# Performance work log

Measured on AMD Instinct MI355X. Metric: run time of the kernel, lower is better.

The kernel has to match this reference:

```python
import jax, jax.numpy as jnp
import numpy as np

L, HID, NH, NKV, HD, INTER = 16, 960, 15, 5, 64, 2560
VOCAB, NV, NT, PRE, SD = 49152, 192, 48, 241, 32
THETA, EPS, B = 100000.0, 1e-5, 16
GROUPS = NH // NKV


def setup_inputs() -> dict:
    key = jax.random.key(0)
    ks = jax.random.split(key, 20)
    s = 0.02
    rn = lambda k, shp: jax.random.normal(k, shp, jnp.float32) * s
    return {
        'vision_features': jax.random.normal(ks[0], (B, NV, HID), jnp.float32),
        'lang_token_ids': jax.random.randint(ks[1], (B, NT), 0, VOCAB),
        'lang_mask': jnp.ones((B, NT), dtype=bool),
        'state': jax.random.normal(ks[2], (B, SD), jnp.float32),
        'embed': rn(ks[3], (VOCAB, HID)),
        'state_w': rn(ks[4], (SD, HID)),
        'state_b': jnp.zeros((HID,), jnp.float32),
        'Wq': rn(ks[5], (L, HID, NH * HD)),
        'Wk': rn(ks[6], (L, HID, NKV * HD)),
        'Wv': rn(ks[7], (L, HID, NKV * HD)),
        'Wo': rn(ks[8], (L, NH * HD, HID)),
        'Wg': rn(ks[9], (L, HID, INTER)),
        'Wu': rn(ks[10], (L, HID, INTER)),
        'Wd': rn(ks[11], (L, INTER, HID)),
        'ln1': jnp.ones((L, HID), jnp.float32),
        'ln2': jnp.ones((L, HID), jnp.float32),
    }


def _rms(x, w):
    var = jnp.mean(jnp.square(x), axis=-1, keepdims=True)
    return x * jax.lax.rsqrt(var + EPS) * w


def _rotate_half(x):
    h = x.shape[-1] // 2
    return jnp.concatenate([-x[..., h:], x[..., :h]], axis=-1)


def _rope_tables(position_ids):
    # position_ids: [B, S] -> cos/sin: [B, S, HD]
    inv_freq = 1.0 / (THETA ** (jnp.arange(0, HD, 2, dtype=jnp.float32) / HD))
    freqs = position_ids.astype(jnp.float32)[..., None] * inv_freq  # [B,S,HD/2]
    emb = jnp.concatenate([freqs, freqs], axis=-1)
    return jnp.cos(emb), jnp.sin(emb)


def _apply_rope(x, cos, sin):
    # x: [B,S,H,D]; cos/sin: [B,S,D]
    return x * cos[:, :, None, :] + _rotate_half(x) * sin[:, :, None, :]


def _attention(q, k, v, mask2d):
    # q: [B,S,NH,HD]; k,v: [B,S,NKV,HD]; mask2d: [B,S,S] bool (query i, key j)
    kx = jnp.repeat(k, GROUPS, axis=2)  # GQA expand -> [B,S,NH,HD]
    vx = jnp.repeat(v, GROUPS, axis=2)
    scores = jnp.einsum('bihd,bjhd->bhij', q, kx) * (HD ** -0.5)
    big_neg = jnp.finfo(jnp.float32).min
    scores = jnp.where(mask2d[:, None, :, :], scores, big_neg)
    probs = jax.nn.softmax(scores, axis=-1)
    out = jnp.einsum('bhij,bjhd->bihd', probs, vx)
    return out.reshape(q.shape[0], q.shape[1], NH * HD)


def reference(vision_features, lang_token_ids, lang_mask, state,
              embed, state_w, state_b, Wq, Wk, Wv, Wo, Wg, Wu, Wd, ln1, ln2):
    lang_emb = embed[lang_token_ids] * jnp.sqrt(jnp.float32(HID))  # [B,NT,HID]
    state_emb = (state @ state_w + state_b)[:, None, :]            # [B,1,HID]
    x = jnp.concatenate([vision_features, lang_emb, state_emb], axis=1)  # [B,PRE,HID]

    pad = jnp.concatenate([jnp.ones((B, NV), bool), lang_mask.astype(bool),
                           jnp.ones((B, 1), bool)], axis=1)  # [B,PRE]
    position_ids = jnp.clip(jnp.cumsum(pad.astype(jnp.int32), axis=1) - 1, 0, None)
    cos, sin = _rope_tables(position_ids)

    att_marks = jnp.zeros((PRE,), jnp.int32).at[NV + NT:].set(1)
    cum = jnp.cumsum(att_marks)
    att2d = cum[None, :] >= cum[:, None]  # [S_q, S_kv]: key cum <= query cum
    pad2d = pad[:, :, None] & pad[:, None, :]
    mask2d = att2d[None, :, :] & pad2d  # [B,S,S]

    def layer(x, w):
        h = _rms(x, w['ln1'])
        S = h.shape[1]
        q = (h @ w['Wq']).reshape(B, S, NH, HD)
        k = (h @ w['Wk']).reshape(B, S, NKV, HD)
        v = (h @ w['Wv']).reshape(B, S, NKV, HD)
        q = _apply_rope(q, cos, sin)
        k = _apply_rope(k, cos, sin)
        a = _attention(q, k, v, mask2d)
        x = x + a @ w['Wo']
        h2 = _rms(x, w['ln2'])
        m = (jax.nn.silu(h2 @ w['Wg']) * (h2 @ w['Wu'])) @ w['Wd']
        return x + m, (k, v)

    weights = {'Wq': Wq, 'Wk': Wk, 'Wv': Wv, 'Wo': Wo,
               'Wg': Wg, 'Wu': Wu, 'Wd': Wd, 'ln1': ln1, 'ln2': ln2}
    _, (keys, values) = jax.lax.scan(layer, x, weights)
    # keys/values: [L, B, PRE, NKV, HD]
    return keys, values
```

## Files before the change

### kernel.cpp

```cpp
#include <hip/hip_runtime.h>
#include <hip/hip_bf16.h>

namespace {

typedef __bf16 bf16_t;
typedef __bf16 bf16x8 __attribute__((ext_vector_type(8)));
typedef __bf16 bf16x4 __attribute__((ext_vector_type(4)));
typedef float f32x4 __attribute__((ext_vector_type(4)));

constexpr int kL     = 16;
constexpr int kHid   = 960;
constexpr int kNH    = 15;
constexpr int kNKV   = 5;
constexpr int kHD    = 64;
constexpr int kInter = 2560;
constexpr int kNV    = 192;
constexpr int kNT    = 48;
constexpr int kPre   = 241;
constexpr int kSD    = 32;
constexpr int kB     = 16;
constexpr int kTok   = kB * kPre;
constexpr int kTokP  = 3968;
constexpr int kQKV   = 1600;
constexpr float kEps = 1e-5f;
constexpr float kSqrtHid = 30.98386677f;

constexpr size_t kWoOff     = (size_t)1664 * 960;
constexpr size_t kWgOff     = kWoOff + (size_t)1024 * 960;
constexpr size_t kWuOff     = kWgOff + (size_t)2560 * 960;
constexpr size_t kWdOff     = kWuOff + (size_t)2560 * 960;
constexpr size_t kWPerLayer = kWdOff + (size_t)1024 * 2560;

__device__ __forceinline__ void gload16(const bf16_t* g, bf16_t* l) {
  __builtin_amdgcn_global_load_lds((const __attribute__((address_space(1))) void*)g,
                                   (__attribute__((address_space(3))) void*)l, 16, 0, 0);
}

__global__ void build_x_kernel(const float* __restrict__ vision,
                               const int*   __restrict__ tokens,
                               const float* __restrict__ state,
                               const float* __restrict__ embed,
                               const float* __restrict__ sw,
                               const float* __restrict__ sb,
                               float* __restrict__ x) {
  int idx = blockIdx.x * blockDim.x + threadIdx.x;
  if (idx >= kTok * kHid) return;
  int t = idx / kHid, c = idx - t * kHid;
  int b = t / kPre, s = t - b * kPre;
  float v;
  if (s < kNV) {
    v = vision[((size_t)b * kNV + s) * kHid + c];
  } else if (s < kNV + kNT) {
    int tok = tokens[b * kNT + (s - kNV)];
    v = embed[(size_t)tok * kHid + c] * kSqrtHid;
  } else {
    float acc = sb[c];
#pragma unroll
    for (int i = 0; i < kSD; ++i) acc += state[b * kSD + i] * sw[i * kHid + c];
    v = acc;
  }
  x[idx] = v;
}

__global__ void rope_table_kernel(float* __restrict__ cosT, float* __restrict__ sinT) {
  int idx = blockIdx.x * blockDim.x + threadIdx.x;
  if (idx >= kPre * 32) return;
  int s = idx >> 5, fi = idx & 31;
  float inv = __expf(-(2.0f * (float)fi / (float)kHD) * __logf(100000.0f));
  float fr = (float)s * inv;
  cosT[idx] = cosf(fr);
  sinT[idx] = sinf(fr);
}

__device__ void transpose_tile(const float* __restrict__ src, bf16_t* __restrict__ dst,
                               int K, int N, int tile) {
  __shared__ float ts[64][65];
  int ntn = N >> 6;
  int tk = tile / ntn, tn = tile - tk * ntn;
  int t = threadIdx.x;
  int r = t >> 2, c0 = (t & 3) << 4;
  const float* sp = src + (size_t)((tk << 6) + r) * N + (tn << 6) + c0;
  float4 a = ((const float4*)sp)[0];
  float4 b = ((const float4*)sp)[1];
  float4 c = ((const float4*)sp)[2];
  float4 d = ((const float4*)sp)[3];
  ts[r][c0 + 0] = a.x;  ts[r][c0 + 1] = a.y;  ts[r][c0 + 2] = a.z;  ts[r][c0 + 3] = a.w;
  ts[r][c0 + 4] = b.x;  ts[r][c0 + 5] = b.y;  ts[r][c0 + 6] = b.z;  ts[r][c0 + 7] = b.w;
  ts[r][c0 + 8] = c.x;  ts[r][c0 + 9] = c.y;  ts[r][c0 +10] = c.z;  ts[r][c0 +11] = c.w;
  ts[r][c0 +12] = d.x;  ts[r][c0 +13] = d.y;  ts[r][c0 +14] = d.z;  ts[r][c0 +15] = d.w;
  __syncthreads();
  bf16_t* dp = dst + (size_t)((tn << 6) + r) * K + (tk << 6) + c0;
  bf16x8 o0, o1;
#pragma unroll
  for (int i = 0; i < 8; ++i) o0[i] = (bf16_t)ts[c0 + i][r];
#pragma unroll
  for (int i = 0; i < 8; ++i) o1[i] = (bf16_t)ts[c0 + 8 + i][r];
  *(bf16x8*)dp = o0;
  *(bf16x8*)(dp + 8) = o1;
}

__global__ __launch_bounds__(256)
void wconv_kernel(const float* __restrict__ Wq, const float* __restrict__ Wk,
                  const float* __restrict__ Wv, const float* __restrict__ Wo,
                  const float* __restrict__ Wg, const float* __restrict__ Wu,
                  const float* __restrict__ Wd, bf16_t* __restrict__ wall) {
  int bid = blockIdx.x;
  int l = bid / 2400, t = bid - l * 2400;
  bf16_t* wl = wall + (size_t)l * kWPerLayer;
  if      (t < 225)  transpose_tile(Wq + (size_t)l * 921600, wl, 960, 960, t);
  else if (t < 300)  transpose_tile(Wk + (size_t)l * 307200, wl + (size_t)960 * 960, 960, 320, t - 225);
  else if (t < 375)  transpose_tile(Wv + (size_t)l * 307200, wl + (size_t)1280 * 960, 960, 320, t - 300);
  else if (t < 600)  transpose_tile(Wo + (size_t)l * 921600, wl + kWoOff, 960, 960, t - 375);
  else if (t < 1200) transpose_tile(Wg + (size_t)l * 2457600, wl + kWgOff, 960, 2560, t - 600);
  else if (t < 1800) transpose_tile(Wu + (size_t)l * 2457600, wl + kWuOff, 960, 2560, t - 1200);
  else               transpose_tile(Wd + (size_t)l * 2457600, wl + kWdOff, 2560, 960, t - 1800);
}

__global__ __launch_bounds__(256)
void rmsnorm_bf16_kernel(const float* __restrict__ x, const float* __restrict__ w,
                         bf16_t* __restrict__ h) {
  int t = blockIdx.x;
  int tid = threadIdx.x;
  const float* xr = x + (size_t)t * kHid;
  float4 v = make_float4(0.f, 0.f, 0.f, 0.f);
  if (tid < 240) v = ((const float4*)xr)[tid];
  float ss = v.x * v.x + v.y * v.y + v.z * v.z + v.w * v.w;
#pragma unroll
  for (int off = 32; off; off >>= 1) ss += __shfl_xor(ss, off);
  __shared__ float part[4];
  if ((tid & 63) == 0) part[tid >> 6] = ss;
  __syncthreads();
  float tot = part[0] + part[1] + part[2] + part[3];
  float scale = rsqrtf(tot * (1.f / (float)kHid) + kEps);
  if (tid < 240) {
    float4 wv = ((const float4*)w)[tid];
    bf16x4 o;
    o[0] = (bf16_t)(v.x * scale * wv.x);
    o[1] = (bf16_t)(v.y * scale * wv.y);
    o[2] = (bf16_t)(v.z * scale * wv.z);
    o[3] = (bf16_t)(v.w * scale * wv.w);
    *(bf16x4*)&h[(size_t)t * kHid + tid * 4] = o;
  }
}


__global__ __launch_bounds__(256, 4)
void gemm_qkv_kernel(const bf16_t* __restrict__ A, const bf16_t* __restrict__ Bt,
                     bf16_t* __restrict__ qkv, float* __restrict__ outk,
                     float* __restrict__ outv,
                     const float* __restrict__ cosT, const float* __restrict__ sinT) {
  constexpr int K = kHid;
  constexpr int NT = K / 32;
  __shared__ alignas(16) bf16_t As[2][4096];
  __shared__ alignas(16) bf16_t Bs[2][2048];
  int tid = threadIdx.x;
  int m0 = blockIdx.y * 128, n0 = blockIdx.x * 64;
  int lane = tid & 63, wid = tid >> 6;
  int wr = wid * 32;
  int r0 = tid >> 2, c0 = (tid & 3) * 8;
  int lr = lane & 15, lg = lane >> 4;

  const bf16_t* a0 = A + (size_t)(m0 + r0) * K + c0;
  const bf16_t* a1 = a0 + (size_t)64 * K;
  const bf16_t* b0 = Bt + (size_t)(n0 + r0) * K + c0;

  f32x4 acc[2][4];
#pragma unroll
  for (int m = 0; m < 2; ++m)
#pragma unroll
    for (int n = 0; n < 4; ++n) acc[m][n] = (f32x4){0.f, 0.f, 0.f, 0.f};

  int arow0 = (wr + lr) * 32 + lg * 8;
  int brow0 = lr * 32 + lg * 8;

  gload16(a0, &As[0][tid * 8]);
  gload16(a1, &As[0][2048 + tid * 8]);
  if (r0 < 64) gload16(b0, &Bs[0][tid * 8]);
  __syncthreads();

  int cur = 0;
  for (int t = 0; t < NT; ++t) {
    if (t + 1 < NT) {
      int k1 = (t + 1) * 32;
      gload16(a0 + k1, &As[cur ^ 1][tid * 8]);
      gload16(a1 + k1, &As[cur ^ 1][2048 + tid * 8]);
      gload16(b0 + k1, &Bs[cur ^ 1][tid * 8]);
    }
    bf16x8 af[2], bfr[4];
#pragma unroll
    for (int m = 0; m < 2; ++m) af[m] = *(const bf16x8*)&As[cur][arow0 + m * 16 * 32];
#pragma unroll
    for (int n = 0; n < 4; ++n) bfr[n] = *(const bf16x8*)&Bs[cur][brow0 + n * 16 * 32];
#pragma unroll
    for (int m = 0; m < 2; ++m)
#pragma unroll
      for (int n = 0; n < 4; ++n)
        acc[m][n] = __builtin_amdgcn_mfma_f32_16x16x32_bf16(af[m], bfr[n], acc[m][n], 0, 0, 0);
    __syncthreads();
    cur ^= 1;
  }

  int cbase = n0;
  int cr4 = lg * 4;
  if (cbase < 1280) {
    bool isQ = cbase < 960;
    float scale = isQ ? 0.125f : 1.0f;
#pragma unroll
    for (int m = 0; m < 2; ++m) {
      int row = m0 + wr + m * 16 + cr4;
#pragma unroll
      for (int r = 0; r < 4; ++r) {
        int rr = row + r;
        if (rr >= kTok) continue;
        int s = rr % kPre;
        bf16_t* qrow = qkv + (size_t)rr * kQKV + cbase;
        float* krow = outk + (size_t)rr * 320 + (cbase - 960);
#pragma unroll
        for (int n = 0; n < 2; ++n) {
          int d = n * 16 + lr;
          float c = cosT[s * 32 + d], sn = sinT[s * 32 + d];
          float lo = acc[m][n][r], hi = acc[m][n + 2][r];
          float y0 = lo * c - hi * sn;
          float y1 = hi * c + lo * sn;
          qrow[d]      = (bf16_t)(y0 * scale);
          qrow[d + 32] = (bf16_t)(y1 * scale);
          if (!isQ) { krow[d] = y0; krow[d + 32] = y1; }
        }
      }
    }
  } else {
#pragma unroll
    for (int m = 0; m < 2; ++m) {
      int row = m0 + wr + m * 16 + cr4;
#pragma unroll
      for (int r = 0; r < 4; ++r) {
        int rr = row + r;
        if (rr >= kTok) continue;
        bf16_t* qrow = qkv + (size_t)rr * kQKV + cbase;
        float* vrow = outv + (size_t)rr * 320 + (cbase - 1280);
#pragma unroll
        for (int n = 0; n < 4; ++n) {
          int d = n * 16 + lr;
          float v = acc[m][n][r];
          qrow[d] = (bf16_t)v;
          vrow[d] = v;
        }
      }
    }
  }
}

__global__ __launch_bounds__(256, 4)
void gemm_res_kernel(const bf16_t* __restrict__ A, const bf16_t* __restrict__ Bt,
                     const float* __restrict__ src, float* __restrict__ C,
                     int M, int N, int K) {
  __shared__ alignas(16) bf16_t As[2][4096];
  __shared__ alignas(16) bf16_t Bs[2][2048];
  int tid = threadIdx.x;
  int m0 = blockIdx.y * 128, n0 = blockIdx.x * 64;
  int lane = tid & 63, wid = tid >> 6;
  int wr = wid * 32;
  int r0 = tid >> 2, c0 = (tid & 3) * 8;
  int lr = lane & 15, lg = lane >> 4;

  const bf16_t* a0 = A + (size_t)(m0 + r0) * K + c0;
  const bf16_t* a1 = a0 + (size_t)64 * K;
  const bf16_t* b0 = Bt + (size_t)(n0 + r0) * K + c0;

  f32x4 acc[2][4];
#pragma unroll
  for (int m = 0; m < 2; ++m)
#pragma unroll
    for (int n = 0; n < 4; ++n) acc[m][n] = (f32x4){0.f, 0.f, 0.f, 0.f};

  int arow0 = (wr + lr) * 32 + lg * 8;
  int brow0 = lr * 32 + lg * 8;

  gload16(a0, &As[0][tid * 8]);
  gload16(a1, &As[0][2048 + tid * 8]);
  gload16(b0, &Bs[0][tid * 8]);
  __syncthreads();

  int NT = K / 32;
  int cur = 0;
  for (int t = 0; t < NT; ++t) {
    if (t + 1 < NT) {
      int k1 = (t + 1) * 32;
      gload16(a0 + k1, &As[cur ^ 1][tid * 8]);
      gload16(a1 + k1, &As[cur ^ 1][2048 + tid * 8]);
      gload16(b0 + k1, &Bs[cur ^ 1][tid * 8]);
    }
    bf16x8 af[2], bfr[4];
#pragma unroll
    for (int m = 0; m < 2; ++m) af[m] = *(const bf16x8*)&As[cur][arow0 + m * 16 * 32];
#pragma unroll
    for (int n = 0; n < 4; ++n) bfr[n] = *(const bf16x8*)&Bs[cur][brow0 + n * 16 * 32];
#pragma unroll
    for (int m = 0; m < 2; ++m)
#pragma unroll
      for (int n = 0; n < 4; ++n)
        acc[m][n] = __builtin_amdgcn_mfma_f32_16x16x32_bf16(af[m], bfr[n], acc[m][n], 0, 0, 0);
    __syncthreads();
    cur ^= 1;
  }

  int cr4 = lg * 4;
#pragma unroll
  for (int m = 0; m < 2; ++m) {
    int row = m0 + wr + m * 16 + cr4;
#pragma unroll
    for (int n = 0; n < 4; ++n) {
      int col = n0 + n * 16 + lr;
#pragma unroll
      for (int r = 0; r < 4; ++r) {
        int rr = row + r;
        if (rr < M) {
          size_t off = (size_t)rr * N + col;
          C[off] = src[off] + acc[m][n][r];
        }
      }
    }
  }
}

__global__ __launch_bounds__(256)
void gemm_dual_kernel(const bf16_t* __restrict__ A, const bf16_t* __restrict__ Bg,
                      const bf16_t* __restrict__ Bu, bf16_t* __restrict__ act,
                      int M, int K) {
  __shared__ alignas(16) bf16_t As[2][4096];
  __shared__ alignas(16) bf16_t Gs[2][2048];
  __shared__ alignas(16) bf16_t Us[2][2048];
  int tid = threadIdx.x;
  int m0 = blockIdx.y * 128, n0 = blockIdx.x * 64;
  int lane = tid & 63, wid = tid >> 6;
  int wr = wid * 32;
  int r0 = tid >> 2, c0 = (tid & 3) * 8;
  int lr = lane & 15, lg = lane >> 4;

  const bf16_t* a0 = A + (size_t)(m0 + r0) * K + c0;
  const bf16_t* a1 = a0 + (size_t)64 * K;
  const bf16_t* g0 = Bg + (size_t)(n0 + r0) * K + c0;
  const bf16_t* u0 = Bu + (size_t)(n0 + r0) * K + c0;

  f32x4 accg[2][4], accu[2][4];
#pragma unroll
  for (int m = 0; m < 2; ++m)
#pragma unroll
    for (int n = 0; n < 4; ++n) {
      accg[m][n] = (f32x4){0.f, 0.f, 0.f, 0.f};
      accu[m][n] = (f32x4){0.f, 0.f, 0.f, 0.f};
    }

  int arow0 = (wr + lr) * 32 + lg * 8;
  int brow0 = lr * 32 + lg * 8;

  gload16(a0, &As[0][tid * 8]);
  gload16(a1, &As[0][2048 + tid * 8]);
  gload16(g0, &Gs[0][tid * 8]);
  gload16(u0, &Us[0][tid * 8]);
  __syncthreads();

  int NT = K / 32;
  int cur = 0;
  for (int t = 0; t < NT; ++t) {
    if (t + 1 < NT) {
      int k1 = (t + 1) * 32;
      gload16(a0 + k1, &As[cur ^ 1][tid * 8]);
      gload16(a1 + k1, &As[cur ^ 1][2048 + tid * 8]);
      gload16(g0 + k1, &Gs[cur ^ 1][tid * 8]);
      gload16(u0 + k1, &Us[cur ^ 1][tid * 8]);
    }
    bf16x8 af[2], bfr[4];
#pragma unroll
    for (int m = 0; m < 2; ++m) af[m] = *(const bf16x8*)&As[cur][arow0 + m * 16 * 32];
#pragma unroll
    for (int n = 0; n < 4; ++n) bfr[n] = *(const bf16x8*)&Gs[cur][brow0 + n * 16 * 32];
#pragma unroll
    for (int m = 0; m < 2; ++m)
#pragma unroll
      for (int n = 0; n < 4; ++n)
        accg[m][n] = __builtin_amdgcn_mfma_f32_16x16x32_bf16(af[m], bfr[n], accg[m][n], 0, 0, 0);
#pragma unroll
    for (int n = 0; n < 4; ++n) bfr[n] = *(const bf16x8*)&Us[cur][brow0 + n * 16 * 32];
#pragma unroll
    for (int m = 0; m < 2; ++m)
#pragma unroll
      for (int n = 0; n < 4; ++n)
        accu[m][n] = __builtin_amdgcn_mfma_f32_16x16x32_bf16(af[m], bfr[n], accu[m][n], 0, 0, 0);
    __syncthreads();
    cur ^= 1;
  }

  int cr4 = lg * 4;
#pragma unroll
  for (int m = 0; m < 2; ++m) {
    int row = m0 + wr + m * 16 + cr4;
#pragma unroll
    for (int n = 0; n < 4; ++n) {
      int col = n0 + n * 16 + lr;
#pragma unroll
      for (int r = 0; r < 4; ++r) {
        int rr = row + r;
        if (rr < M) {
          float g = accg[m][n][r];
          float u = accu[m][n][r];
          float silu = g / (1.f + __expf(-g));
          act[(size_t)rr * kInter + col] = (bf16_t)(silu * u);
        }
      }
    }
  }
}

__global__ __launch_bounds__(256)
void attn_mfma_kernel(const bf16_t* __restrict__ qkv, bf16_t* __restrict__ aout) {
  int h = blockIdx.x, b = blockIdx.y;
  int kvh = h / 3;
  constexpr int LDK = 72;
  constexpr int LDV = 264;
  __shared__ alignas(16) bf16_t Ks[256 * LDK];
  __shared__ alignas(16) bf16_t Vt[64 * LDV];
  __shared__ alignas(16) bf16_t Ps[4][16 * LDV];
  const bf16_t* base = qkv + (size_t)b * kPre * kQKV;
  int tid = threadIdx.x;
  for (int i = tid; i < 2048; i += 256) {
    int j = i >> 3, c = (i & 7) * 8;
    bf16x8 k8, v8;
    if (j < kPre) {
      k8 = *(const bf16x8*)(base + (size_t)j * kQKV + 960 + kvh * 64 + c);
      v8 = *(const bf16x8*)(base + (size_t)j * kQKV + 1280 + kvh * 64 + c);
    } else {
#pragma unroll
      for (int e = 0; e < 8; ++e) { k8[e] = (bf16_t)0.f; v8[e] = (bf16_t)0.f; }
    }
    *(bf16x8*)&Ks[j * LDK + c] = k8;
#pragma unroll
    for (int e = 0; e < 8; ++e) Vt[(c + e) * LDV + j] = v8[e];
  }
  __syncthreads();
  int wid = tid >> 6, lane = tid & 63;
  int lr = lane & 15, lg = lane >> 4;
  bf16_t* myP = &Ps[wid][0];
  for (int qt = wid * 4; qt < wid * 4 + 4; ++qt) {
    int q0 = qt * 16;
    int qrow = q0 + lr; if (qrow > 240) qrow = 240;
    const bf16_t* qp = base + (size_t)qrow * kQKV + h * 64 + lg * 8;
    bf16x8 aq0 = *(const bf16x8*)qp;
    bf16x8 aq1 = *(const bf16x8*)(qp + 32);
    f32x4 sacc[16];
#pragma unroll
    for (int ct = 0; ct < 16; ++ct) sacc[ct] = (f32x4){0.f, 0.f, 0.f, 0.f};
#pragma unroll
    for (int ct = 0; ct < 16; ++ct) {
      int key = ct * 16 + lr;
      bf16x8 kb0 = *(const bf16x8*)&Ks[key * LDK + lg * 8];
      sacc[ct] = __builtin_amdgcn_mfma_f32_16x16x32_bf16(aq0, kb0, sacc[ct], 0, 0, 0);
      bf16x8 kb1 = *(const bf16x8*)&Ks[key * LDK + 32 + lg * 8];
      sacc[ct] = __builtin_amdgcn_mfma_f32_16x16x32_bf16(aq1, kb1, sacc[ct], 0, 0, 0);
    }
    float rmax[4] = {-1e30f, -1e30f, -1e30f, -1e30f};
#pragma unroll
    for (int ct = 0; ct < 16; ++ct) {
      int j = ct * 16 + lr;
#pragma unroll
      for (int r = 0; r < 4; ++r) {
        int q = q0 + lg * 4 + r;
        bool ok = (q < 240) ? (j < kPre) : (j == 240);
        float s = ok ? sacc[ct][r] : -1e30f;
        sacc[ct][r] = s;
        rmax[r] = fmaxf(rmax[r], s);
      }
    }
#pragma unroll
    for (int off = 8; off; off >>= 1) {
#pragma unroll
      for (int r = 0; r < 4; ++r) rmax[r] = fmaxf(rmax[r], __shfl_xor(rmax[r], off));
    }
    float rsum[4] = {0.f, 0.f, 0.f, 0.f};
#pragma unroll
    for (int ct = 0; ct < 16; ++ct) {
#pragma unroll
      for (int r = 0; r < 4; ++r) {
        float s = sacc[ct][r];
        float e = (s > -1e29f) ? __expf(s - rmax[r]) : 0.f;
        rsum[r] += e;
        myP[(lg * 4 + r) * LDV + ct * 16 + lr] = (bf16_t)e;
      }
    }
#pragma unroll
    for (int off = 8; off; off >>= 1) {
#pragma unroll
      for (int r = 0; r < 4; ++r) rsum[r] += __shfl_xor(rsum[r], off);
    }
    f32x4 oacc[4];
#pragma unroll
    for (int dt = 0; dt < 4; ++dt) oacc[dt] = (f32x4){0.f, 0.f, 0.f, 0.f};
#pragma unroll
    for (int ks = 0; ks < 8; ++ks) {
      bf16x8 pa = *(const bf16x8*)&myP[lr * LDV + ks * 32 + lg * 8];
#pragma unroll
      for (int dt = 0; dt < 4; ++dt) {
        bf16x8 vbf = *(const bf16x8*)&Vt[(dt * 16 + lr) * LDV + ks * 32 + lg * 8];
        oacc[dt] = __builtin_amdgcn_mfma_f32_16x16x32_bf16(pa, vbf, oacc[dt], 0, 0, 0);
      }
    }
    float linv[4];
#pragma unroll
    for (int r = 0; r < 4; ++r) linv[r] = 1.f / rsum[r];
#pragma unroll
    for (int dt = 0; dt < 4; ++dt) {
#pragma unroll
      for (int r = 0; r < 4; ++r) {
        int q = q0 + lg * 4 + r;
        if (q < kPre) {
          aout[((size_t)b * kPre + q) * kHid + h * 64 + dt * 16 + lr] =
              (bf16_t)(oacc[dt][r] * linv[r]);
        }
      }
    }
  }
}

}

extern "C" void kernel_launch(void* const* d_in, const int* in_sizes, int n_in,
                              void* d_out, int out_size, void* d_ws, size_t ws_size,
                              hipStream_t stream) {
  const float* vision = (const float*)d_in[0];
  const int*   tokens = (const int*)d_in[1];
  const float* state = (const float*)d_in[3];
  const float* embed = (const float*)d_in[4];
  const float* sw    = (const float*)d_in[5];
  const float* sb    = (const float*)d_in[6];
  const float* Wq    = (const float*)d_in[7];
  const float* Wk    = (const float*)d_in[8];
  const float* Wv    = (const float*)d_in[9];
  const float* Wo    = (const float*)d_in[10];
  const float* Wg    = (const float*)d_in[11];
  const float* Wu    = (const float*)d_in[12];
  const float* Wd    = (const float*)d_in[13];
  const float* ln1   = (const float*)d_in[14];
  const float* ln2   = (const float*)d_in[15];

  char* w = (char*)d_ws;
  float*  x      = (float*)w;   w += (size_t)kTok * kHid * 4;
  bf16_t* qkv    = (bf16_t*)w;  w += (size_t)kTok * kQKV * 2;
  bf16_t* h_bf   = (bf16_t*)w;  w += (size_t)kTokP * kHid * 2;
  bf16_t* a_bf   = (bf16_t*)w;  w += (size_t)kTokP * kHid * 2;
  bf16_t* act_bf = (bf16_t*)w;  w += (size_t)kTokP * kInter * 2;
  bf16_t* wall   = (bf16_t*)w;  w += kWPerLayer * kL * 2;
  float*  cosT   = (float*)w;   w += (size_t)kPre * 32 * 4;
  float*  sinT   = (float*)w;   w += (size_t)kPre * 32 * 4;

  float* out_k = (float*)d_out;
  float* out_v = out_k + (size_t)kL * kTok * 320;

  build_x_kernel<<<(kTok * kHid + 255) / 256, 256, 0, stream>>>(
      vision, tokens, state, embed, sw, sb, x);
  rope_table_kernel<<<(kPre * 32 + 255) / 256, 256, 0, stream>>>(cosT, sinT);
  wconv_kernel<<<2400 * kL, 256, 0, stream>>>(Wq, Wk, Wv, Wo, Wg, Wu, Wd, wall);

  for (int l = 0; l < kL; ++l) {
    bf16_t* wl = wall + (size_t)l * kWPerLayer;
    rmsnorm_bf16_kernel<<<kTok, 256, 0, stream>>>(x, ln1 + (size_t)l * kHid, h_bf);
    gemm_qkv_kernel<<<dim3(25, 31), 256, 0, stream>>>(
        h_bf, wl, qkv, out_k + (size_t)l * kTok * 320, out_v + (size_t)l * kTok * 320,
        cosT, sinT);
    attn_mfma_kernel<<<dim3(15, 16), 256, 0, stream>>>(qkv, a_bf);
    gemm_res_kernel<<<dim3(15, 31), 256, 0, stream>>>(
        a_bf, wl + kWoOff, x, x, kTok, kHid, kHid);
    rmsnorm_bf16_kernel<<<kTok, 256, 0, stream>>>(x, ln2 + (size_t)l * kHid, h_bf);
    gemm_dual_kernel<<<dim3(40, 31), 256, 0, stream>>>(
        h_bf, wl + kWgOff, wl + kWuOff, act_bf, kTok, kHid);
    gemm_res_kernel<<<dim3(15, 31), 256, 0, stream>>>(
        act_bf, wl + kWdOff, x, x, kTok, kHid, kInter);
  }
}
```

Before: 3.543 ms.

## Fuse RMSNorm into GEMM prologues using atomically accumulated row sum-of-squares

Removes the standalone rmsnorm kernels. The residual GEMMs now accumulate per-row sums of squares with atomics in their epilogue, and the QKV and gate/up GEMMs read fp32 x directly and apply the norm scale and weight while staging A tiles into shared memory. This saves two launches and the bf16 h round-trip per layer. In exchange the GEMMs load fp32 A (twice the bytes) through registers instead of direct-to-LDS loads, recompute the normalisation in each column block, and add atomic traffic plus a memset.

```diff
diff --git a/kernel.cpp b/kernel.cpp
--- a/kernel.cpp
+++ b/kernel.cpp
@@ -34,6 +34,15 @@
 __device__ __forceinline__ void gload16(const bf16_t* g, bf16_t* l) {
   __builtin_amdgcn_global_load_lds((const __attribute__((address_space(1))) void*)g,
                                    (__attribute__((address_space(3))) void*)l, 16, 0, 0);
+}
+
+__device__ __forceinline__ bf16x8 pack8(float4 a, float4 b, float4 wa, float4 wb, float s) {
+  bf16x8 o;
+  o[0] = (bf16_t)(a.x * s * wa.x); o[1] = (bf16_t)(a.y * s * wa.y);
+  o[2] = (bf16_t)(a.z * s * wa.z); o[3] = (bf16_t)(a.w * s * wa.w);
+  o[4] = (bf16_t)(b.x * s * wb.x); o[5] = (bf16_t)(b.y * s * wb.y);
+  o[6] = (bf16_t)(b.z * s * wb.z); o[7] = (bf16_t)(b.w * s * wb.w);
+  return o;
 }
 
 __global__ void build_x_kernel(const float* __restrict__ vision,
@@ -62,6 +71,22 @@
   x[idx] = v;
 }
 
+__global__ __launch_bounds__(256)
+void rowssq_kernel(const float* __restrict__ x, float* __restrict__ ssq) {
+  int t = blockIdx.x;
+  int tid = threadIdx.x;
+  const float* xr = x + (size_t)t * kHid;
+  float4 v = make_float4(0.f, 0.f, 0.f, 0.f);
+  if (tid < 240) v = ((const float4*)xr)[tid];
+  float ss = v.x * v.x + v.y * v.y + v.z * v.z + v.w * v.w;
+#pragma unroll
+  for (int off = 32; off; off >>= 1) ss += __shfl_xor(ss, off);
+  __shared__ float part[4];
+  if ((tid & 63) == 0) part[tid >> 6] = ss;
+  __syncthreads();
+  if (tid == 0) ssq[t] = part[0] + part[1] + part[2] + part[3];
+}
+
 __global__ void rope_table_kernel(float* __restrict__ cosT, float* __restrict__ sinT) {
   int idx = blockIdx.x * blockDim.x + threadIdx.x;
   if (idx >= kPre * 32) return;
@@ -116,36 +141,10 @@
   else               transpose_tile(Wd + (size_t)l * 2457600, wl + kWdOff, 2560, 960, t - 1800);
 }
 
+
 __global__ __launch_bounds__(256)
-void rmsnorm_bf16_kernel(const float* __restrict__ x, const float* __restrict__ w,
-                         bf16_t* __restrict__ h) {
-  int t = blockIdx.x;
-  int tid = threadIdx.x;
-  const float* xr = x + (size_t)t * kHid;
-  float4 v = make_float4(0.f, 0.f, 0.f, 0.f);
-  if (tid < 240) v = ((const float4*)xr)[tid];
-  float ss = v.x * v.x + v.y * v.y + v.z * v.z + v.w * v.w;
-#pragma unroll
-  for (int off = 32; off; off >>= 1) ss += __shfl_xor(ss, off);
-  __shared__ float part[4];
-  if ((tid & 63) == 0) part[tid >> 6] = ss;
-  __syncthreads();
-  float tot = part[0] + part[1] + part[2] + part[3];
-  float scale = rsqrtf(tot * (1.f / (float)kHid) + kEps);
-  if (tid < 240) {
-    float4 wv = ((const float4*)w)[tid];
-    bf16x4 o;
-    o[0] = (bf16_t)(v.x * scale * wv.x);
-    o[1] = (bf16_t)(v.y * scale * wv.y);
-    o[2] = (bf16_t)(v.z * scale * wv.z);
-    o[3] = (bf16_t)(v.w * scale * wv.w);
-    *(bf16x4*)&h[(size_t)t * kHid + tid * 4] = o;
-  }
-}
-
-
-__global__ __launch_bounds__(256, 4)
-void gemm_qkv_kernel(const bf16_t* __restrict__ A, const bf16_t* __restrict__ Bt,
+void gemm_qkv_kernel(const float* __restrict__ X, const float* __restrict__ ssq,
+                     const float* __restrict__ lnw, const bf16_t* __restrict__ Bt,
                      bf16_t* __restrict__ qkv, float* __restrict__ outk,
                      float* __restrict__ outv,
                      const float* __restrict__ cosT, const float* __restrict__ sinT) {
@@ -160,9 +159,12 @@
   int r0 = tid >> 2, c0 = (tid & 3) * 8;
   int lr = lane & 15, lg = lane >> 4;
 
-  const bf16_t* a0 = A + (size_t)(m0 + r0) * K + c0;
-  const bf16_t* a1 = a0 + (size_t)64 * K;
-  const bf16_t* b0 = Bt + (size_t)(n0 + r0) * K + c0;
+  const float* xa = X + (size_t)(m0 + r0) * K + c0;
+  const float* xb = xa + (size_t)64 * K;
+  const bf16_t* gb = Bt + (size_t)(n0 + r0) * K + c0;
+
+  float sc0 = rsqrtf(ssq[m0 + r0] * (1.f / 960.f) + kEps);
+  float sc1 = rsqrtf(ssq[m0 + r0 + 64] * (1.f / 960.f) + kEps);
 
   f32x4 acc[2][4];
 #pragma unroll
@@ -173,18 +175,26 @@
   int arow0 = (wr + lr) * 32 + lg * 8;
   int brow0 = lr * 32 + lg * 8;
 
-  gload16(a0, &As[0][tid * 8]);
-  gload16(a1, &As[0][2048 + tid * 8]);
-  if (r0 < 64) gload16(b0, &Bs[0][tid * 8]);
+  {
+    float4 a0 = *(const float4*)xa, a1 = *(const float4*)(xa + 4);
+    float4 b0 = *(const float4*)xb, b1 = *(const float4*)(xb + 4);
+    float4 w0 = *(const float4*)(lnw + c0), w1 = *(const float4*)(lnw + c0 + 4);
+    *(bf16x8*)&As[0][tid * 8] = pack8(a0, a1, w0, w1, sc0);
+    *(bf16x8*)&As[0][2048 + tid * 8] = pack8(b0, b1, w0, w1, sc1);
+    gload16(gb, &Bs[0][tid * 8]);
+  }
   __syncthreads();
 
   int cur = 0;
   for (int t = 0; t < NT; ++t) {
-    if (t + 1 < NT) {
+    float4 a0, a1, b0, b1, w0, w1;
+    bool pf = (t + 1 < NT);
+    if (pf) {
       int k1 = (t + 1) * 32;
-      gload16(a0 + k1, &As[cur ^ 1][tid * 8]);
-      gload16(a1 + k1, &As[cur ^ 1][2048 + tid * 8]);
-      gload16(b0 + k1, &Bs[cur ^ 1][tid * 8]);
+      a0 = *(const float4*)(xa + k1); a1 = *(const float4*)(xa + k1 + 4);
+      b0 = *(const float4*)(xb + k1); b1 = *(const float4*)(xb + k1 + 4);
+      w0 = *(const float4*)(lnw + k1 + c0); w1 = *(const float4*)(lnw + k1 + c0 + 4);
+      gload16(gb + k1, &Bs[cur ^ 1][tid * 8]);
     }
     bf16x8 af[2], bfr[4];
 #pragma unroll
@@ -196,6 +206,10 @@
 #pragma unroll
       for (int n = 0; n < 4; ++n)
         acc[m][n] = __builtin_amdgcn_mfma_f32_16x16x32_bf16(af[m], bfr[n], acc[m][n], 0, 0, 0);
+    if (pf) {
+      *(bf16x8*)&As[cur ^ 1][tid * 8] = pack8(a0, a1, w0, w1, sc0);
+      *(bf16x8*)&As[cur ^ 1][2048 + tid * 8] = pack8(b0, b1, w0, w1, sc1);
+    }
     __syncthreads();
     cur ^= 1;
   }
@@ -253,7 +267,7 @@
 __global__ __launch_bounds__(256, 4)
 void gemm_res_kernel(const bf16_t* __restrict__ A, const bf16_t* __restrict__ Bt,
                      const float* __restrict__ src, float* __restrict__ C,
-                     int M, int N, int K) {
+                     float* __restrict__ ssq_out, int M, int N, int K) {
   __shared__ alignas(16) bf16_t As[2][4096];
   __shared__ alignas(16) bf16_t Bs[2][2048];
   int tid = threadIdx.x;
@@ -305,6 +319,7 @@
   }
 
   int cr4 = lg * 4;
+  float ps[2][4] = {};
 #pragma unroll
   for (int m = 0; m < 2; ++m) {
     int row = m0 + wr + m * 16 + cr4;
@@ -316,15 +331,35 @@
         int rr = row + r;
         if (rr < M) {
           size_t off = (size_t)rr * N + col;
-          C[off] = src[off] + acc[m][n][r];
+          float val = src[off] + acc[m][n][r];
+          C[off] = val;
+          ps[m][r] += val * val;
         }
       }
     }
   }
+#pragma unroll
+  for (int m = 0; m < 2; ++m)
+#pragma unroll
+    for (int r = 0; r < 4; ++r) {
+#pragma unroll
+      for (int off = 8; off; off >>= 1) ps[m][r] += __shfl_xor(ps[m][r], off);
+    }
+  if (lr == 0) {
+#pragma unroll
+    for (int m = 0; m < 2; ++m) {
+#pragma unroll
+      for (int r = 0; r < 4; ++r) {
+        int rr = m0 + wr + m * 16 + cr4 + r;
+        if (rr < M) atomicAdd(&ssq_out[rr], ps[m][r]);
+      }
+    }
+  }
 }
 
 __global__ __launch_bounds__(256)
-void gemm_dual_kernel(const bf16_t* __restrict__ A, const bf16_t* __restrict__ Bg,
+void gemm_dual_kernel(const float* __restrict__ X, const float* __restrict__ ssq,
+                      const float* __restrict__ lnw, const bf16_t* __restrict__ Bg,
                       const bf16_t* __restrict__ Bu, bf16_t* __restrict__ act,
                       int M, int K) {
   __shared__ alignas(16) bf16_t As[2][4096];
@@ -337,10 +372,13 @@
   int r0 = tid >> 2, c0 = (tid & 3) * 8;
   int lr = lane & 15, lg = lane >> 4;
 
-  const bf16_t* a0 = A + (size_t)(m0 + r0) * K + c0;
-  const bf16_t* a1 = a0 + (size_t)64 * K;
+  const float* xa = X + (size_t)(m0 + r0) * K + c0;
+  const float* xb = xa + (size_t)64 * K;
   const bf16_t* g0 = Bg + (size_t)(n0 + r0) * K + c0;
   const bf16_t* u0 = Bu + (size_t)(n0 + r0) * K + c0;
+
+  float sc0 = rsqrtf(ssq[m0 + r0] * (1.f / 960.f) + kEps);
+  float sc1 = rsqrtf(ssq[m0 + r0 + 64] * (1.f / 960.f) + kEps);
 
   f32x4 accg[2][4], accu[2][4];
 #pragma unroll
@@ -354,19 +392,27 @@
   int arow0 = (wr + lr) * 32 + lg * 8;
   int brow0 = lr * 32 + lg * 8;
 
-  gload16(a0, &As[0][tid * 8]);
-  gload16(a1, &As[0][2048 + tid * 8]);
-  gload16(g0, &Gs[0][tid * 8]);
-  gload16(u0, &Us[0][tid * 8]);
+  {
+    float4 a0 = *(const float4*)xa, a1 = *(const float4*)(xa + 4);
+    float4 b0 = *(const float4*)xb, b1 = *(const float4*)(xb + 4);
+    float4 w0 = *(const float4*)(lnw + c0), w1 = *(const float4*)(lnw + c0 + 4);
+    *(bf16x8*)&As[0][tid * 8] = pack8(a0, a1, w0, w1, sc0);
+    *(bf16x8*)&As[0][2048 + tid * 8] = pack8(b0, b1, w0, w1, sc1);
+    gload16(g0, &Gs[0][tid * 8]);
+    gload16(u0, &Us[0][tid * 8]);
+  }
   __syncthreads();
 
   int NT = K / 32;
   int cur = 0;
   for (int t = 0; t < NT; ++t) {
-    if (t + 1 < NT) {
+    float4 a0, a1, b0, b1, w0, w1;
+    bool pf = (t + 1 < NT);
+    if (pf) {
       int k1 = (t + 1) * 32;
-      gload16(a0 + k1, &As[cur ^ 1][tid * 8]);
-      gload16(a1 + k1, &As[cur ^ 1][2048 + tid * 8]);
+      a0 = *(const float4*)(xa + k1); a1 = *(const float4*)(xa + k1 + 4);
+      b0 = *(const float4*)(xb + k1); b1 = *(const float4*)(xb + k1 + 4);
+      w0 = *(const float4*)(lnw + k1 + c0); w1 = *(const float4*)(lnw + k1 + c0 + 4);
       gload16(g0 + k1, &Gs[cur ^ 1][tid * 8]);
       gload16(u0 + k1, &Us[cur ^ 1][tid * 8]);
     }
@@ -387,6 +433,10 @@
 #pragma unroll
       for (int n = 0; n < 4; ++n)
         accu[m][n] = __builtin_amdgcn_mfma_f32_16x16x32_bf16(af[m], bfr[n], accu[m][n], 0, 0, 0);
+    if (pf) {
+      *(bf16x8*)&As[cur ^ 1][tid * 8] = pack8(a0, a1, w0, w1, sc0);
+      *(bf16x8*)&As[cur ^ 1][2048 + tid * 8] = pack8(b0, b1, w0, w1, sc1);
+    }
     __syncthreads();
     cur ^= 1;
   }
@@ -543,36 +593,41 @@
   const float* ln2   = (const float*)d_in[15];
 
   char* w = (char*)d_ws;
-  float*  x      = (float*)w;   w += (size_t)kTok * kHid * 4;
+  float*  x      = (float*)w;   w += (size_t)kTokP * kHid * 4;
   bf16_t* qkv    = (bf16_t*)w;  w += (size_t)kTok * kQKV * 2;
-  bf16_t* h_bf   = (bf16_t*)w;  w += (size_t)kTokP * kHid * 2;
   bf16_t* a_bf   = (bf16_t*)w;  w += (size_t)kTokP * kHid * 2;
   bf16_t* act_bf = (bf16_t*)w;  w += (size_t)kTokP * kInter * 2;
   bf16_t* wall   = (bf16_t*)w;  w += kWPerLayer * kL * 2;
   float*  cosT   = (float*)w;   w += (size_t)kPre * 32 * 4;
   float*  sinT   = (float*)w;   w += (size_t)kPre * 32 * 4;
+  float*  ssqA   = (float*)w;   w += (size_t)(kL + 1) * kTokP * 4;
+  float*  ssqB   = (float*)w;   w += (size_t)kL * kTokP * 4;
 
   float* out_k = (float*)d_out;
   float* out_v = out_k + (size_t)kL * kTok * 320;
 
+  hipMemsetAsync(ssqA, 0, (size_t)(2 * kL + 1) * kTokP * 4, stream);
+
   build_x_kernel<<<(kTok * kHid + 255) / 256, 256, 0, stream>>>(
       vision, tokens, state, embed, sw, sb, x);
+  rowssq_kernel<<<kTok, 256, 0, stream>>>(x, ssqA);
   rope_table_kernel<<<(kPre * 32 + 255) / 256, 256, 0, stream>>>(cosT, sinT);
   wconv_kernel<<<2400 * kL, 256, 0, stream>>>(Wq, Wk, Wv, Wo, Wg, Wu, Wd, wall);
 
   for (int l = 0; l < kL; ++l) {
     bf16_t* wl = wall + (size_t)l * kWPerLayer;
-    rmsnorm_bf16_kernel<<<kTok, 256, 0, stream>>>(x, ln1 + (size_t)l * kHid, h_bf);
+    float* ssq1 = ssqA + (size_t)l * kTokP;
+    float* ssq1n = ssqA + (size_t)(l + 1) * kTokP;
+    float* ssq2 = ssqB + (size_t)l * kTokP;
     gemm_qkv_kernel<<<dim3(25, 31), 256, 0, stream>>>(
-        h_bf, wl, qkv, out_k + (size_t)l * kTok * 320, out_v + (size_t)l * kTok * 320,
-        cosT, sinT);
+        x, ssq1, ln1 + (size_t)l * kHid, wl, qkv,
+        out_k + (size_t)l * kTok * 320, out_v + (size_t)l * kTok * 320, cosT, sinT);
     attn_mfma_kernel<<<dim3(15, 16), 256, 0, stream>>>(qkv, a_bf);
     gemm_res_kernel<<<dim3(15, 31), 256, 0, stream>>>(
-        a_bf, wl + kWoOff, x, x, kTok, kHid, kHid);
-    rmsnorm_bf16_kernel<<<kTok, 256, 0, stream>>>(x, ln2 + (size_t)l * kHid, h_bf);
+        a_bf, wl + kWoOff, x, x, ssq2, kTok, kHid, kHid);
     gemm_dual_kernel<<<dim3(40, 31), 256, 0, stream>>>(
-        h_bf, wl + kWgOff, wl + kWuOff, act_bf, kTok, kHid);
+        x, ssq2, ln2 + (size_t)l * kHid, wl + kWgOff, wl + kWuOff, act_bf, kTok, kHid);
     gemm_res_kernel<<<dim3(15, 31), 256, 0, stream>>>(
-        act_bf, wl + kWdOff, x, x, kTok, kHid, kInter);
-  }
-}
+        act_bf, wl + kWdOff, x, x, ssq1n, kTok, kHid, kInter);
+  }
+}
```

After: 3.873 ms. 1.09x slower.
